# Optimization experiments

Hardware: AMD Instinct MI355X
Metric: run time of the kernel (lower is better)

The kernel has to match this reference:

```python
import jax, jax.numpy as jnp
import numpy as np
import math

E, N, K, R = 1024, 16, 4, 64  # embed_dim, state_dim, d_conv, dt_rank=ceil(E/16)
B, L = 2, 2048


def setup_inputs() -> dict:
    key = jax.random.key(0)
    ks = jax.random.split(key, 8)
    gn = lambda k, sh, sc: jax.random.normal(k, sh, dtype=jnp.float32) * sc
    W_z = gn(ks[0], (E, E), E ** -0.5)                      # in_proj_z weight (no bias)
    W_params = gn(ks[1], (R + 2 * N, E), E ** -0.5)         # in_proj_params weight (no bias)
    conv_w = gn(ks[2], (E, 1, K), 0.5)                      # depthwise conv1d weight, no bias
    dt_std = R ** -0.5 * 0.1
    W_dt = jax.random.uniform(ks[3], (E, R), jnp.float32, -dt_std, dt_std)
    b_dt = jnp.full((E,), math.log(math.expm1(0.001)), dtype=jnp.float32)
    A_log = jnp.tile(jnp.log(jnp.arange(1, N + 1, dtype=jnp.float32))[None, :], (E, 1))
    D = jnp.ones((E,), dtype=jnp.float32)
    W_out = gn(ks[4], (E, E), E ** -0.5)
    x = jax.random.normal(ks[5], (B, L, E), dtype=jnp.float32)
    return dict(x=x, W_z=W_z, W_params=W_params, conv_w=conv_w, W_dt=W_dt,
                b_dt=b_dt, A_log=A_log, D=D, W_out=W_out)


def reference(x, W_z, W_params, conv_w, W_dt, b_dt, A_log, D, W_out):
    b, l, e = x.shape
    n = A_log.shape[1]
    r = W_dt.shape[1]
    k = conv_w.shape[-1]

    z = x @ W_z.T                                           # [B,L,E]
    params = x @ W_params.T                                 # [B,L,R+2N]
    dt_unproj = params[..., :r]
    # B_proj = params[..., r:r+n] is computed but UNUSED in the original forward
    C_proj = params[..., r + n:]                            # [B,L,N]
    dt = jax.nn.softplus(dt_unproj @ W_dt.T + b_dt)         # [B,L,E]

    # depthwise causal conv: torch pads K-1 both sides then slices [:L] == left-pad K-1
    xc = jax.lax.conv_general_dilated(
        x.transpose(0, 2, 1), conv_w, (1,), [(k - 1, 0)],
        dimension_numbers=('NCH', 'OIH', 'NCH'), feature_group_count=e)
    u = jax.nn.silu(xc.transpose(0, 2, 1))                  # [B,L,E]

    A = -jnp.exp(A_log)                                     # [E,N]
    A_tilde = jnp.exp(dt[..., None] * A[None, None])        # [B,L,E,N]
    B_tilde = jnp.where(jnp.abs(A)[None, None] < 1e-5,
                        dt[..., None],
                        (A_tilde - 1.0) / (A[None, None] + 1e-10))

    # recurrence (note t-1 indexing, faithful to original):
    # h_0 = B~[0]*u[0];  h_t = A~[t-1]*h_{t-1} + B~[t-1]*u[t-1]
    h0 = B_tilde[:, 0] * u[:, 0, :, None]                   # [B,E,N]

    def step(h, inp):
        a, bt, uu = inp
        h_new = a * h + bt * uu[..., None]
        return h_new, h_new

    xs = (A_tilde[:, :-1].transpose(1, 0, 2, 3),
          B_tilde[:, :-1].transpose(1, 0, 2, 3),
          u[:, :-1].transpose(1, 0, 2))
    _, hs = jax.lax.scan(step, h0, xs)                      # [L-1,B,E,N]
    h = jnp.concatenate([h0[None], hs], axis=0).transpose(1, 0, 2, 3)  # [B,L,E,N]

    y = jnp.einsum('bln,blen->ble', C_proj, h)
    y_ssm = y + u * D
    y_gated = y_ssm * jax.nn.silu(z)
    return y_gated @ W_out.T
```

## Files before the change

### kernel.cpp

```cpp
#include <hip/hip_runtime.h>
#include <math.h>

#define B_ 2
#define L_ 2048
#define E_ 1024
#define N_ 16
#define R_ 64
#define PWP 128
#define BL_ (B_*L_)

using bf16x8 = __attribute__((ext_vector_type(8))) short;
using f32x4  = __attribute__((ext_vector_type(4))) float;

__device__ __forceinline__ float softplusf(float x) {
    return fmaxf(x, 0.0f) + log1pf(expf(-fabsf(x)));
}
__device__ __forceinline__ float siluf(float x) {
    return x / (1.0f + expf(-x));
}
__device__ __forceinline__ ushort f2bf(float f) {
    unsigned u = __float_as_uint(f);
    return (ushort)((u + 0x7fffu + ((u >> 16) & 1u)) >> 16);
}
__device__ __forceinline__ float bf2f(ushort h) {
    return __uint_as_float(((unsigned)h) << 16);
}
__device__ __forceinline__ void gload16(const ushort* g, ushort* l) {
    __builtin_amdgcn_global_load_lds((const __attribute__((address_space(1))) void*)g,
                                     (__attribute__((address_space(3))) void*)l, 16, 0, 0);
}

__device__ __forceinline__ void split_body(const float* __restrict__ src, int spitch,
                                           int rows_src, ushort* __restrict__ dst,
                                           int K, int total4, int idx) {
    if (idx >= total4) return;
    const int Kq = K >> 2;
    const int r  = idx / Kq;
    const int c4 = (idx - r * Kq) << 2;
    float f[4] = {0.f, 0.f, 0.f, 0.f};
    if (r < rows_src)
        *reinterpret_cast<float4*>(f) = *reinterpret_cast<const float4*>(src + (size_t)r * spitch + c4);
    ushort h[4], lo[4];
#pragma unroll
    for (int q = 0; q < 4; ++q) {
        h[q]  = f2bf(f[q]);
        lo[q] = f2bf(f[q] - bf2f(h[q]));
    }
    ushort* d0 = dst + (size_t)r * 2 * K + c4;
    *reinterpret_cast<uint2*>(d0)     = make_uint2((uint)h[0]  | ((uint)h[1]  << 16), (uint)h[2]  | ((uint)h[3]  << 16));
    *reinterpret_cast<uint2*>(d0 + K) = make_uint2((uint)lo[0] | ((uint)lo[1] << 16), (uint)lo[2] | ((uint)lo[3] << 16));
}

__global__ __launch_bounds__(256)
void split_rm(const float* __restrict__ src, int spitch, int rows_src,
              ushort* __restrict__ dst, int K, int total4) {
    split_body(src, spitch, rows_src, dst, K, total4, blockIdx.x * 256 + threadIdx.x);
}

__global__ __launch_bounds__(256)
void split_w3(const float* __restrict__ Wz, const float* __restrict__ Wp,
              const float* __restrict__ Wdt, ushort* __restrict__ WzC,
              ushort* __restrict__ WpC, ushort* __restrict__ WdtC) {
    const int idx = blockIdx.x * 256 + threadIdx.x;
    if (blockIdx.y == 0)      split_body(Wz,  E_, E_,  WzC,  E_, E_ * E_ / 4, idx);
    else if (blockIdx.y == 1) split_body(Wp,  E_, 96,  WpC,  E_, 128 * E_ / 4, idx);
    else                      split_body(Wdt, R_, E_,  WdtC, R_, E_ * R_ / 4, idx);
}

__global__ __launch_bounds__(256)
void split_tr(const float* __restrict__ ygT, ushort* __restrict__ Ycat) {
    __shared__ float Ts[64][65];
    const int e0 = blockIdx.x * 64;
    const int l0 = blockIdx.y * 64;
    const int b  = blockIdx.z;
    const int tid = threadIdx.x;
    for (int idx = tid; idx < 64 * 64; idx += 256) {
        const int rr = idx >> 6, cc = idx & 63;
        Ts[rr][cc] = ygT[((size_t)(b * E_ + e0 + rr) << 11) + l0 + cc];
    }
    __syncthreads();
    for (int idx = tid; idx < 64 * 16; idx += 256) {
        const int rl = idx >> 4, g = idx & 15;
        ushort h[4], lo[4];
#pragma unroll
        for (int q = 0; q < 4; ++q) {
            const float f = Ts[g * 4 + q][rl];
            h[q]  = f2bf(f);
            lo[q] = f2bf(f - bf2f(h[q]));
        }
        ushort* d0 = Ycat + (size_t)(b * L_ + l0 + rl) * 2 * E_ + e0 + g * 4;
        *reinterpret_cast<uint2*>(d0)      = make_uint2((uint)h[0]  | ((uint)h[1]  << 16), (uint)h[2]  | ((uint)h[3]  << 16));
        *reinterpret_cast<uint2*>(d0 + E_) = make_uint2((uint)lo[0] | ((uint)lo[1] << 16), (uint)lo[2] | ((uint)lo[3] << 16));
    }
}

template<int BM, int BN, int BK, int MODE>
__global__ __launch_bounds__(256)
void mfma_gemm(const ushort* __restrict__ A, const ushort* __restrict__ Bm,
               const float* __restrict__ bias, ushort* __restrict__ P2,
               float* __restrict__ C, int Kd, int Ncols) {
    constexpr int WTM = BM / 2, WTN = BN / 2;
    constexpr int MI = WTM / 16, NJ = WTN / 16;
    constexpr int CPR = BK / 8;
    constexpr int KS  = BK / 32;
    constexpr int RPW = 64 / CPR;
    __shared__ ushort As[BM * BK];
    __shared__ ushort Bs[BN * BK];
    const int tid  = threadIdx.x;
    const int wave = tid >> 6, lane = tid & 63;
    const int m0 = blockIdx.x * BM, n0 = blockIdx.y * BN;
    const int wr = wave >> 1, wc = wave & 1;
    const int fr = lane & 15, fg = lane >> 4;
    const int kxor = (fr & 7) << 3;
    const int pK = 2 * Kd;

    f32x4 acc[MI][NJ];
#pragma unroll
    for (int i = 0; i < MI; ++i)
#pragma unroll
        for (int j = 0; j < NJ; ++j) { f32x4 z = {0.f, 0.f, 0.f, 0.f}; acc[i][j] = z; }

    const int lrow = lane / CPR;
    const int lc   = lane % CPR;

    const int KP = Kd / BK;
    for (int seg = 0; seg < 3; ++seg) {
        const int ao = (seg == 2) ? Kd : 0;
        const int bo = (seg == 1) ? Kd : 0;
        for (int tt = 0; tt < KP; ++tt) {
            const int ka = ao + tt * BK, kb = bo + tt * BK;
#pragma unroll
            for (int g = 0; g < BM / (4 * RPW); ++g) {
                const int srow = (wave * (BM / (4 * RPW)) + g) * RPW + lrow;
                const int sc = (lc & 8) | ((lc ^ (srow & 7)) & 7);
                gload16(A + (size_t)(m0 + srow) * pK + ka + sc * 8, As + srow * BK + lc * 8);
            }
#pragma unroll
            for (int g = 0; g < BN / (4 * RPW); ++g) {
                const int srow = (wave * (BN / (4 * RPW)) + g) * RPW + lrow;
                const int sc = (lc & 8) | ((lc ^ (srow & 7)) & 7);
                gload16(Bm + (size_t)(n0 + srow) * pK + kb + sc * 8, Bs + srow * BK + lc * 8);
            }
            __syncthreads();

#pragma unroll
            for (int ks = 0; ks < KS; ++ks) {
                bf16x8 av[MI], bv[NJ];
#pragma unroll
                for (int i = 0; i < MI; ++i) {
                    const int row = wr * WTM + i * 16 + fr;
                    av[i] = *reinterpret_cast<const bf16x8*>(&As[row * BK + ((ks * 32 + fg * 8) ^ kxor)]);
                }
#pragma unroll
                for (int j = 0; j < NJ; ++j) {
                    const int row = wc * WTN + j * 16 + fr;
                    bv[j] = *reinterpret_cast<const bf16x8*>(&Bs[row * BK + ((ks * 32 + fg * 8) ^ kxor)]);
                }
#pragma unroll
                for (int i = 0; i < MI; ++i)
#pragma unroll
                    for (int j = 0; j < NJ; ++j)
                        acc[i][j] = __builtin_amdgcn_mfma_f32_16x16x32_bf16(av[i], bv[j], acc[i][j], 0, 0, 0);
            }
            __syncthreads();
        }
    }

    if constexpr (MODE == 0) {
#pragma unroll
        for (int i = 0; i < MI; ++i) {
            const int m = m0 + wr * WTM + i * 16 + fg * 4;
#pragma unroll
            for (int j = 0; j < NJ; ++j) {
                const int n = n0 + wc * WTN + j * 16 + fr;
#pragma unroll
                for (int r = 0; r < 4; ++r)
                    C[(size_t)(m + r) * Ncols + n] = acc[i][j][r];
            }
        }
    } else if constexpr (MODE == 3) {
#pragma unroll
        for (int i = 0; i < MI; ++i) {
            const int m = m0 + wr * WTM + i * 16 + fg * 4;
#pragma unroll
            for (int j = 0; j < NJ; ++j) {
                const int n = n0 + wc * WTN + j * 16 + fr;
#pragma unroll
                for (int r = 0; r < 4; ++r) {
                    const float v = acc[i][j][r];
                    const int mm = m + r;
                    if (n < 64) {
                        const ushort hh = f2bf(v);
                        P2[(size_t)mm * 128 + n]      = hh;
                        P2[(size_t)mm * 128 + 64 + n] = f2bf(v - bf2f(hh));
                    } else if (n >= 80 && n < 96) {
                        C[(size_t)mm * Ncols + n] = v;
                    }
                }
            }
        }
    } else {
        const int b  = n0 >> 11;
        const int lb = n0 - (b << 11);
#pragma unroll
        for (int i = 0; i < MI; ++i) {
            const int e = m0 + wr * WTM + i * 16 + fg * 4;
#pragma unroll
            for (int r = 0; r < 4; ++r) {
                const float bia = (MODE == 2) ? bias[e + r] : 0.0f;
                float* row = C + ((size_t)(b * E_ + e + r) << 11) + lb;
#pragma unroll
                for (int j = 0; j < NJ; ++j) {
                    float v = acc[i][j][r];
                    if constexpr (MODE == 2) v = softplusf(v + bia);
                    row[wc * WTN + j * 16 + fr] = v;
                }
            }
        }
    }
}

__global__ __launch_bounds__(256)
void conv_silu_kernel(const float* __restrict__ x, const float* __restrict__ cw,
                      float* __restrict__ uT) {
    __shared__ float Xt[67][65];
    const int e0 = blockIdx.x * 64;
    const int l0 = blockIdx.y * 64;
    const int b  = blockIdx.z;
    const int tid = threadIdx.x;
    for (int idx = tid; idx < 67 * 64; idx += 256) {
        const int row = idx >> 6, col = idx & 63;
        const int gl = l0 - 3 + row;
        Xt[row][col] = (gl >= 0) ? x[((size_t)b * L_ + gl) * E_ + e0 + col] : 0.0f;
    }
    __syncthreads();
    const int lL = tid & 63;
    const int w  = tid >> 6;
    for (int ee = w; ee < 64; ee += 4) {
        const int e = e0 + ee;
        const float w0 = cw[e*4+0], w1 = cw[e*4+1], w2 = cw[e*4+2], w3 = cw[e*4+3];
        const float v = w0*Xt[lL][ee] + w1*Xt[lL+1][ee] + w2*Xt[lL+2][ee] + w3*Xt[lL+3][ee];
        uT[((size_t)b * E_ + e) * L_ + l0 + lL] = siluf(v);
    }
}

__global__ __launch_bounds__(256)
void scan_kernel(const float* __restrict__ dtT, const float* __restrict__ uT,
                 const float* __restrict__ zT, const float* __restrict__ params,
                 const float* __restrict__ A_log, const float* __restrict__ Dp,
                 float* __restrict__ ygT) {
    __shared__ float sdt[64 * 33];
    __shared__ float su [64 * 33];
    __shared__ float sz [64 * 33];
    __shared__ float wPs[4][N_];
    __shared__ float wLs[4][N_];
    const int c = blockIdx.x;
    const int b = c >> 10;
    const int e = c & (E_ - 1);
    const int tid  = threadIdx.x;
    const int wave = tid >> 6, lane = tid & 63;
    constexpr int CH = 8;
    constexpr float LOG2E = 1.44269504088896340736f;

    const float* dtp = dtT + ((size_t)b * E_ + e) * L_;
    const float* up  = uT  + ((size_t)b * E_ + e) * L_;
    const float* zp  = zT  + ((size_t)b * E_ + e) * L_;

#pragma unroll
    for (int it = 0; it < 2; ++it) {
        const int l = (it * 256 + tid) * 4;
        const int slot = ((l >> 5) * 33) + (l & 31);
        float4 vd = *reinterpret_cast<const float4*>(dtp + l);
        float4 vu = *reinterpret_cast<const float4*>(up  + l);
        float4 vz = *reinterpret_cast<const float4*>(zp  + l);
        sdt[slot] = vd.x; sdt[slot+1] = vd.y; sdt[slot+2] = vd.z; sdt[slot+3] = vd.w;
        su [slot] = vu.x; su [slot+1] = vu.y; su [slot+2] = vu.z; su [slot+3] = vu.w;
        sz [slot] = vz.x; sz [slot+1] = vz.y; sz [slot+2] = vz.z; sz [slot+3] = vz.w;
    }

    float An2[N_], rA[N_];
    unsigned selm = 0;
#pragma unroll
    for (int n = 0; n < N_; ++n) {
        const float A = -expf(A_log[e * N_ + n]);
        An2[n] = A * LOG2E;
        if (fabsf(A) < 1e-5f) selm |= (1u << n);
        rA[n] = 1.0f / (A + 1e-10f);
    }
    const float Dv = Dp[e];
    __syncthreads();

    const int base = (tid >> 2) * 33 + (tid & 3) * 8;
    const float d0 = sdt[0];
    const float u0 = su[0];

    float P[N_], h[N_];
#pragma unroll
    for (int n = 0; n < N_; ++n) { P[n] = 1.0f; h[n] = 0.0f; }
#pragma unroll
    for (int j = 0; j < CH; ++j) {
        const float d  = sdt[base + j];
        const float uu = su [base + j];
#pragma unroll
        for (int n = 0; n < N_; ++n) {
            const float at = __builtin_amdgcn_exp2f(d * An2[n]);
            const float bt = ((selm >> n) & 1u) ? d : (at - 1.0f) * rA[n];
            h[n] = fmaf(at, h[n], bt * uu);
            P[n] *= at;
        }
    }

#pragma unroll
    for (int off = 1; off < 64; off <<= 1) {
#pragma unroll
        for (int n = 0; n < N_; ++n) {
            const float Pp = __shfl_up(P[n], off);
            const float Lp = __shfl_up(h[n], off);
            if (lane >= off) {
                h[n] = fmaf(P[n], Lp, h[n]);
                P[n] *= Pp;
            }
        }
    }

    if (lane == 63) {
#pragma unroll
        for (int n = 0; n < N_; ++n) { wPs[wave][n] = P[n]; wLs[wave][n] = h[n]; }
    }
    float cP[N_], cL[N_];
#pragma unroll
    for (int n = 0; n < N_; ++n) {
        cP[n] = __shfl_up(P[n], 1);
        cL[n] = __shfl_up(h[n], 1);
    }
    __syncthreads();

    float EP[N_], EL[N_];
#pragma unroll
    for (int n = 0; n < N_; ++n) { EP[n] = 1.0f; EL[n] = 0.0f; }
    for (int w2 = 0; w2 < wave; ++w2) {
#pragma unroll
        for (int n = 0; n < N_; ++n) {
            EL[n] = fmaf(wPs[w2][n], EL[n], wLs[w2][n]);
            EP[n] *= wPs[w2][n];
        }
    }
#pragma unroll
    for (int n = 0; n < N_; ++n) {
        const float pl = (lane == 0) ? 1.0f : cP[n];
        const float ll = (lane == 0) ? 0.0f : cL[n];
        const float fP = pl * EP[n];
        const float fL = fmaf(pl, EL[n], ll);
        const float at0 = __builtin_amdgcn_exp2f(d0 * An2[n]);
        const float bt0 = ((selm >> n) & 1u) ? d0 : (at0 - 1.0f) * rA[n];
        const float g0  = bt0 * u0;
        h[n] = fmaf(fP, g0, fL);
    }

    const float* crow = params + (size_t)b * L_ * PWP + 80;
    const int l0 = tid * CH;
#pragma unroll
    for (int j = 0; j < CH; ++j) {
        const float d  = sdt[base + j];
        const float uu = su [base + j];
        const float zv = sz [base + j];
        float Cv[N_];
        const float4* Cp4 = reinterpret_cast<const float4*>(crow + (size_t)(l0 + j) * PWP);
#pragma unroll
        for (int t = 0; t < N_ / 4; ++t)
            *reinterpret_cast<float4*>(Cv + t * 4) = Cp4[t];
        float y = 0.0f;
#pragma unroll
        for (int n = 0; n < N_; ++n) y = fmaf(Cv[n], h[n], y);
        const float outv = (y + uu * Dv) * siluf(zv);
        if (j < CH - 1) {
#pragma unroll
            for (int n = 0; n < N_; ++n) {
                const float at = __builtin_amdgcn_exp2f(d * An2[n]);
                const float bt = ((selm >> n) & 1u) ? d : (at - 1.0f) * rA[n];
                h[n] = fmaf(at, h[n], bt * uu);
            }
        }
        sz[base + j] = outv;
    }
    __syncthreads();

    float* yp = ygT + ((size_t)b * E_ + e) * L_;
#pragma unroll
    for (int it = 0; it < 2; ++it) {
        const int l = (it * 256 + tid) * 4;
        const int slot = ((l >> 5) * 33) + (l & 31);
        float4 o;
        o.x = sz[slot]; o.y = sz[slot+1]; o.z = sz[slot+2]; o.w = sz[slot+3];
        *reinterpret_cast<float4*>(yp + l) = o;
    }
}

extern "C" void kernel_launch(void* const* d_in, const int* in_sizes, int n_in,
                              void* d_out, int out_size, void* d_ws, size_t ws_size,
                              hipStream_t stream) {
    const float* x     = (const float*)d_in[0];
    const float* W_z   = (const float*)d_in[1];
    const float* W_p   = (const float*)d_in[2];
    const float* cw    = (const float*)d_in[3];
    const float* W_dt  = (const float*)d_in[4];
    const float* b_dt  = (const float*)d_in[5];
    const float* A_log = (const float*)d_in[6];
    const float* Dp    = (const float*)d_in[7];
    const float* W_out = (const float*)d_in[8];
    float* out = (float*)d_out;

    char* w = (char*)d_ws;
    ushort* Xcat   = (ushort*)(w);
    ushort* Wzcat  = (ushort*)(w + 16777216);
    ushort* Wpcat  = (ushort*)(w + 20971520);
    ushort* Wdtcat = (ushort*)(w + 21495808);
    ushort* Pcat   = (ushort*)(w + 21757952);
    float*  params = (float*)(w + 22806528);
    float*  zT     = (float*)(w + 24903680);
    float*  dtT    = (float*)(w + 41680896);
    float*  uT     = (float*)(w + 58458112);
    float*  ygT    = (float*)(w + 75235328);
    ushort* Ycat   = Xcat;
    ushort* Wocat  = Wzcat;

    split_rm<<<4096, 256, 0, stream>>>(x, E_, BL_, Xcat, E_, BL_ * E_ / 4);
    split_w3<<<dim3(1024, 3), 256, 0, stream>>>(W_z, W_p, W_dt, Wzcat, Wpcat, Wdtcat);
    mfma_gemm<128,64,128,1><<<dim3(E_ / 128, BL_ / 64), 256, 0, stream>>>(
        Wzcat, Xcat, nullptr, nullptr, zT, E_, 0);
    mfma_gemm<64,64,128,3><<<dim3(BL_ / 64, 2), 256, 0, stream>>>(
        Xcat, Wpcat, nullptr, Pcat, params, E_, PWP);
    mfma_gemm<128,64,64,2><<<dim3(E_ / 128, BL_ / 64), 256, 0, stream>>>(
        Wdtcat, Pcat, b_dt, nullptr, dtT, R_, 0);
    conv_silu_kernel<<<dim3(E_ / 64, L_ / 64, B_), 256, 0, stream>>>(x, cw, uT);
    scan_kernel<<<B_ * E_, 256, 0, stream>>>(dtT, uT, zT, params, A_log, Dp, ygT);
    split_tr<<<dim3(E_ / 64, L_ / 64, B_), 256, 0, stream>>>(ygT, Ycat);
    split_rm<<<1024, 256, 0, stream>>>(W_out, E_, E_, Wocat, E_, E_ * E_ / 4);
    mfma_gemm<128,64,128,0><<<dim3(BL_ / 128, E_ / 64), 256, 0, stream>>>(
        Ycat, Wocat, nullptr, nullptr, out, E_, E_);
}
```

Baseline: 291.6 us.

## Fuse conv with bf16 split of x and restructure scan to two waves

Merges the depthwise conv+SiLU kernel with the bf16 hi/lo split of x, so x is read from global memory once instead of twice and one launch is removed. The scan kernel moves from four waves to two, each thread handling 16 steps, which cuts the cross-wave combine down to a single carry. z is no longer staged in shared memory; z and the C rows are prefetched one step ahead directly from global memory. The trade-off is fewer threads per block and a longer sequential chunk per thread, which may lower occupancy and lengthen the serial dependency chain.

```diff
diff --git a/kernel.cpp b/kernel.cpp
--- a/kernel.cpp
+++ b/kernel.cpp
@@ -221,8 +221,8 @@
 }
 
 __global__ __launch_bounds__(256)
-void conv_silu_kernel(const float* __restrict__ x, const float* __restrict__ cw,
-                      float* __restrict__ uT) {
+void conv_split_kernel(const float* __restrict__ x, const float* __restrict__ cw,
+                       float* __restrict__ uT, ushort* __restrict__ Xcat) {
     __shared__ float Xt[67][65];
     const int e0 = blockIdx.x * 64;
     const int l0 = blockIdx.y * 64;
@@ -242,24 +242,35 @@
         const float v = w0*Xt[lL][ee] + w1*Xt[lL+1][ee] + w2*Xt[lL+2][ee] + w3*Xt[lL+3][ee];
         uT[((size_t)b * E_ + e) * L_ + l0 + lL] = siluf(v);
     }
-}
-
-__global__ __launch_bounds__(256)
+    for (int idx = tid; idx < 64 * 16; idx += 256) {
+        const int rl = idx >> 4, g = idx & 15;
+        ushort h[4], lo[4];
+#pragma unroll
+        for (int q = 0; q < 4; ++q) {
+            const float f = Xt[3 + rl][g * 4 + q];
+            h[q]  = f2bf(f);
+            lo[q] = f2bf(f - bf2f(h[q]));
+        }
+        ushort* d0 = Xcat + (size_t)(b * L_ + l0 + rl) * 2 * E_ + e0 + g * 4;
+        *reinterpret_cast<uint2*>(d0)      = make_uint2((uint)h[0]  | ((uint)h[1]  << 16), (uint)h[2]  | ((uint)h[3]  << 16));
+        *reinterpret_cast<uint2*>(d0 + E_) = make_uint2((uint)lo[0] | ((uint)lo[1] << 16), (uint)lo[2] | ((uint)lo[3] << 16));
+    }
+}
+
+__global__ __launch_bounds__(128)
 void scan_kernel(const float* __restrict__ dtT, const float* __restrict__ uT,
                  const float* __restrict__ zT, const float* __restrict__ params,
                  const float* __restrict__ A_log, const float* __restrict__ Dp,
                  float* __restrict__ ygT) {
     __shared__ float sdt[64 * 33];
     __shared__ float su [64 * 33];
-    __shared__ float sz [64 * 33];
-    __shared__ float wPs[4][N_];
-    __shared__ float wLs[4][N_];
+    __shared__ float wP1[N_], wL1[N_];
     const int c = blockIdx.x;
     const int b = c >> 10;
     const int e = c & (E_ - 1);
     const int tid  = threadIdx.x;
     const int wave = tid >> 6, lane = tid & 63;
-    constexpr int CH = 8;
+    constexpr int CH = 16;
     constexpr float LOG2E = 1.44269504088896340736f;
 
     const float* dtp = dtT + ((size_t)b * E_ + e) * L_;
@@ -267,15 +278,13 @@
     const float* zp  = zT  + ((size_t)b * E_ + e) * L_;
 
 #pragma unroll
-    for (int it = 0; it < 2; ++it) {
-        const int l = (it * 256 + tid) * 4;
+    for (int it = 0; it < 4; ++it) {
+        const int l = (it * 128 + tid) * 4;
         const int slot = ((l >> 5) * 33) + (l & 31);
         float4 vd = *reinterpret_cast<const float4*>(dtp + l);
         float4 vu = *reinterpret_cast<const float4*>(up  + l);
-        float4 vz = *reinterpret_cast<const float4*>(zp  + l);
         sdt[slot] = vd.x; sdt[slot+1] = vd.y; sdt[slot+2] = vd.z; sdt[slot+3] = vd.w;
         su [slot] = vu.x; su [slot+1] = vu.y; su [slot+2] = vu.z; su [slot+3] = vu.w;
-        sz [slot] = vz.x; sz [slot+1] = vz.y; sz [slot+2] = vz.z; sz [slot+3] = vz.w;
     }
 
     float An2[N_], rA[N_];
@@ -290,14 +299,14 @@
     const float Dv = Dp[e];
     __syncthreads();
 
-    const int base = (tid >> 2) * 33 + (tid & 3) * 8;
+    const int base = (tid >> 1) * 33 + (tid & 1) * 16;
     const float d0 = sdt[0];
     const float u0 = su[0];
 
     float P[N_], h[N_];
 #pragma unroll
     for (int n = 0; n < N_; ++n) { P[n] = 1.0f; h[n] = 0.0f; }
-#pragma unroll
+#pragma unroll 4
     for (int j = 0; j < CH; ++j) {
         const float d  = sdt[base + j];
         const float uu = su [base + j];
@@ -323,9 +332,9 @@
         }
     }
 
-    if (lane == 63) {
-#pragma unroll
-        for (int n = 0; n < N_; ++n) { wPs[wave][n] = P[n]; wLs[wave][n] = h[n]; }
+    if (wave == 0 && lane == 63) {
+#pragma unroll
+        for (int n = 0; n < N_; ++n) { wP1[n] = P[n]; wL1[n] = h[n]; }
     }
     float cP[N_], cL[N_];
 #pragma unroll
@@ -335,22 +344,13 @@
     }
     __syncthreads();
 
-    float EP[N_], EL[N_];
-#pragma unroll
-    for (int n = 0; n < N_; ++n) { EP[n] = 1.0f; EL[n] = 0.0f; }
-    for (int w2 = 0; w2 < wave; ++w2) {
-#pragma unroll
-        for (int n = 0; n < N_; ++n) {
-            EL[n] = fmaf(wPs[w2][n], EL[n], wLs[w2][n]);
-            EP[n] *= wPs[w2][n];
-        }
-    }
 #pragma unroll
     for (int n = 0; n < N_; ++n) {
         const float pl = (lane == 0) ? 1.0f : cP[n];
         const float ll = (lane == 0) ? 0.0f : cL[n];
-        const float fP = pl * EP[n];
-        const float fL = fmaf(pl, EL[n], ll);
+        float fP, fL;
+        if (wave == 0) { fP = pl; fL = ll; }
+        else           { fP = pl * wP1[n]; fL = fmaf(pl, wL1[n], ll); }
         const float at0 = __builtin_amdgcn_exp2f(d0 * An2[n]);
         const float bt0 = ((selm >> n) & 1u) ? d0 : (at0 - 1.0f) * rA[n];
         const float g0  = bt0 * u0;
@@ -359,20 +359,32 @@
 
     const float* crow = params + (size_t)b * L_ * PWP + 80;
     const int l0 = tid * CH;
+    float4 pc0, pc1, pc2, pc3;
+    {
+        const float4* Cp4 = reinterpret_cast<const float4*>(crow + (size_t)l0 * PWP);
+        pc0 = Cp4[0]; pc1 = Cp4[1]; pc2 = Cp4[2]; pc3 = Cp4[3];
+    }
+    float pz = zp[l0];
 #pragma unroll
     for (int j = 0; j < CH; ++j) {
+        float4 nc0, nc1, nc2, nc3; float nz = 0.0f;
+        if (j < CH - 1) {
+            const float4* Np = reinterpret_cast<const float4*>(crow + (size_t)(l0 + j + 1) * PWP);
+            nc0 = Np[0]; nc1 = Np[1]; nc2 = Np[2]; nc3 = Np[3];
+            nz = zp[l0 + j + 1];
+        }
         const float d  = sdt[base + j];
         const float uu = su [base + j];
-        const float zv = sz [base + j];
-        float Cv[N_];
-        const float4* Cp4 = reinterpret_cast<const float4*>(crow + (size_t)(l0 + j) * PWP);
-#pragma unroll
-        for (int t = 0; t < N_ / 4; ++t)
-            *reinterpret_cast<float4*>(Cv + t * 4) = Cp4[t];
         float y = 0.0f;
-#pragma unroll
-        for (int n = 0; n < N_; ++n) y = fmaf(Cv[n], h[n], y);
-        const float outv = (y + uu * Dv) * siluf(zv);
+        y = fmaf(pc0.x, h[0],  y); y = fmaf(pc0.y, h[1],  y);
+        y = fmaf(pc0.z, h[2],  y); y = fmaf(pc0.w, h[3],  y);
+        y = fmaf(pc1.x, h[4],  y); y = fmaf(pc1.y, h[5],  y);
+        y = fmaf(pc1.z, h[6],  y); y = fmaf(pc1.w, h[7],  y);
+        y = fmaf(pc2.x, h[8],  y); y = fmaf(pc2.y, h[9],  y);
+        y = fmaf(pc2.z, h[10], y); y = fmaf(pc2.w, h[11], y);
+        y = fmaf(pc3.x, h[12], y); y = fmaf(pc3.y, h[13], y);
+        y = fmaf(pc3.z, h[14], y); y = fmaf(pc3.w, h[15], y);
+        const float outv = (y + uu * Dv) * siluf(pz);
         if (j < CH - 1) {
 #pragma unroll
             for (int n = 0; n < N_; ++n) {
@@ -381,17 +393,18 @@
                 h[n] = fmaf(at, h[n], bt * uu);
             }
         }
-        sz[base + j] = outv;
+        sdt[base + j] = outv;
+        pc0 = nc0; pc1 = nc1; pc2 = nc2; pc3 = nc3; pz = nz;
     }
     __syncthreads();
 
     float* yp = ygT + ((size_t)b * E_ + e) * L_;
 #pragma unroll
-    for (int it = 0; it < 2; ++it) {
-        const int l = (it * 256 + tid) * 4;
+    for (int it = 0; it < 4; ++it) {
+        const int l = (it * 128 + tid) * 4;
         const int slot = ((l >> 5) * 33) + (l & 31);
         float4 o;
-        o.x = sz[slot]; o.y = sz[slot+1]; o.z = sz[slot+2]; o.w = sz[slot+3];
+        o.x = sdt[slot]; o.y = sdt[slot+1]; o.z = sdt[slot+2]; o.w = sdt[slot+3];
         *reinterpret_cast<float4*>(yp + l) = o;
     }
 }
@@ -424,7 +437,7 @@
     ushort* Ycat   = Xcat;
     ushort* Wocat  = Wzcat;
 
-    split_rm<<<4096, 256, 0, stream>>>(x, E_, BL_, Xcat, E_, BL_ * E_ / 4);
+    conv_split_kernel<<<dim3(E_ / 64, L_ / 64, B_), 256, 0, stream>>>(x, cw, uT, Xcat);
     split_w3<<<dim3(1024, 3), 256, 0, stream>>>(W_z, W_p, W_dt, Wzcat, Wpcat, Wdtcat);
     mfma_gemm<128,64,128,1><<<dim3(E_ / 128, BL_ / 64), 256, 0, stream>>>(
         Wzcat, Xcat, nullptr, nullptr, zT, E_, 0);
@@ -432,8 +445,7 @@
         Xcat, Wpcat, nullptr, Pcat, params, E_, PWP);
     mfma_gemm<128,64,64,2><<<dim3(E_ / 128, BL_ / 64), 256, 0, stream>>>(
         Wdtcat, Pcat, b_dt, nullptr, dtT, R_, 0);
-    conv_silu_kernel<<<dim3(E_ / 64, L_ / 64, B_), 256, 0, stream>>>(x, cw, uT);
-    scan_kernel<<<B_ * E_, 256, 0, stream>>>(dtT, uT, zT, params, A_log, Dp, ygT);
+    scan_kernel<<<B_ * E_, 128, 0, stream>>>(dtT, uT, zT, params, A_log, Dp, ygT);
     split_tr<<<dim3(E_ / 64, L_ / 64, B_), 256, 0, stream>>>(ygT, Ycat);
     split_rm<<<1024, 256, 0, stream>>>(W_out, E_, E_, Wocat, E_, E_ * E_ / 4);
     mfma_gemm<128,64,128,0><<<dim3(BL_ / 128, E_ / 64), 256, 0, stream>>>(
```

Result: no change. 294.6 us (+1.0%).
